# Kernel optimization log

Measured on AMD Instinct MI355X. Metric: run time of the kernel, lower is better.

## Reference

```python
import jax, jax.numpy as jnp
import numpy as np

B, S, H = 32, 1024, 1024
W, K = 128, 6
NUM_HEADS = 16


def setup_inputs() -> dict:
    key = jax.random.key(0)
    k1, k2 = jax.random.split(key, 2)
    token_embeddings = jax.random.normal(k1, (B, S, H), dtype=jnp.float32)
    # nn.MultiheadAttention packed in_proj (q,k,v). v / out_proj never affect the
    # module output (attn_output is discarded), but we keep full-size params.
    in_proj_weight = jax.random.normal(k2, (3 * H, H), dtype=jnp.float32) * (1.0 / np.sqrt(H))
    in_proj_bias = jnp.zeros((3 * H,), dtype=jnp.float32)
    # Build ragged word->subtoken map as padded [B, W, K] indices + validity mask.
    # Words occupy disjoint contiguous slots (stride S//W = 8 >= K), matching the
    # disjointness the tokenizer guarantees in get_subtok_map.
    rng = np.random.default_rng(0)
    lengths = rng.integers(2, K + 1, size=(B, W))  # each kept word has >=2 subtokens
    stride = S // W
    base = (np.arange(W) * stride)[None, :, None] + np.arange(K)[None, None, :]
    base = np.broadcast_to(base, (B, W, K))
    mask = np.arange(K)[None, None, :] < lengths[:, :, None]
    idx = np.where(mask, base, 0)
    return {
        "token_embeddings": token_embeddings,
        "in_proj_weight": in_proj_weight,
        "in_proj_bias": in_proj_bias,
        "subtok_idx": jnp.asarray(idx, dtype=jnp.int32),
        "subtok_mask": jnp.asarray(mask),
        "num_heads": NUM_HEADS,
    }


def _merge(token_embeddings, in_proj_weight, in_proj_bias, subtok_idx, subtok_mask, num_heads):
    Bv, Sv, Hv = token_embeddings.shape
    Wv, Kv = subtok_idx.shape[1], subtok_idx.shape[2]
    hd = Hv // num_heads
    dtype = token_embeddings.dtype
    maskf = subtok_mask.astype(dtype)
    b_idx = jnp.arange(Bv)[:, None, None]
    sub = token_embeddings[b_idx, subtok_idx]                      # [B,W,K,H] gather
    x = (sub * maskf[..., None]).reshape(Bv * Wv, Kv, Hv)          # zero-padded groups
    # q,k projections (v / out_proj do not influence returned embeddings)
    qk = x @ in_proj_weight[: 2 * Hv].T + in_proj_bias[: 2 * Hv]
    q, k = qk[..., :Hv], qk[..., Hv:]
    q = q.reshape(-1, Kv, num_heads, hd).transpose(0, 2, 1, 3)     # [L,nh,K,hd]
    k = k.reshape(-1, Kv, num_heads, hd).transpose(0, 2, 1, 3)
    scores = jnp.einsum('lnqd,lnkd->lnqk', q, k) / jnp.asarray(np.sqrt(hd), dtype)
    m = maskf.reshape(-1, Kv)
    pair = m[:, :, None] * m[:, None, :]                           # [L,K,K] 0/1 float mask
    # torch adds float attn_mask to scores (it does NOT -inf mask here) -- faithful
    scores = scores + pair[:, None]
    attn = jax.nn.softmax(scores, axis=-1)
    w_mean = attn.mean(axis=1)                                     # avg over heads (need_weights)
    contrib = (pair * w_mean).sum(axis=1)                          # sum over query dim
    contrib = contrib / (contrib.sum(axis=-1, keepdims=True) + 1e-8)
    contrib = contrib.reshape(Bv, Wv, Kv)                          # zero at invalid k
    unified = jnp.einsum('bwkh,bwk->bwh', sub, contrib)
    # zero ALL subtoken positions of each word, then write merged vector at the
    # first subtoken index (equivalent to the torch in-place per-word loop since
    # word index sets are disjoint). Column Sv is a discard slot for padding.
    safe_idx = jnp.where(subtok_mask, subtok_idx, Sv)
    keep = jnp.ones((Bv, Sv + 1), dtype=dtype)
    keep = keep.at[b_idx, safe_idx].set(0.0)
    out = token_embeddings * keep[:, :Sv, None]
    out = jnp.concatenate([out, jnp.zeros((Bv, 1, Hv), dtype)], axis=1)
    first_idx = jnp.where(subtok_mask[:, :, 0], subtok_idx[:, :, 0], Sv)
    out = out.at[jnp.arange(Bv)[:, None], first_idx].set(unified)
    return out[:, :Sv]


def reference(token_embeddings, in_proj_weight, in_proj_bias, subtok_idx, subtok_mask, num_heads):
    return _merge(token_embeddings, in_proj_weight, in_proj_bias, subtok_idx, subtok_mask, num_heads)
```

## Files before the change

### kernel.cpp

```cpp
#include <hip/hip_runtime.h>
#include <hip/hip_bf16.h>
#include <stdint.h>
#include <stddef.h>

#define Bdim  32
#define Sdim  1024
#define Hdim  1024
#define Wdim  128
#define Ktok  6
#define NHEAD 16
#define HDdim 64
#define Lgrp  (Bdim*Wdim)
#define Mrows (Lgrp*Ktok)
#define Ncols (2*Hdim)
#define CVTROWS (Mrows + Ncols)

#define BMg 256
#define BNg 256
#define BKg 64
#define NKT (Hdim/BKg)

typedef __attribute__((ext_vector_type(8))) short short8;
typedef __attribute__((ext_vector_type(4))) short short4_t;
typedef __attribute__((ext_vector_type(4))) float floatx4;
typedef __hip_bfloat16 bf16_t;

typedef unsigned int u32_g __attribute__((address_space(1)));
typedef unsigned int u32_l __attribute__((address_space(3)));

__device__ __forceinline__ void gld_lds16(const void* g, void* l) {
    __builtin_amdgcn_global_load_lds((const u32_g*)g, (u32_l*)l, 16, 0, 0);
}

__device__ __forceinline__ float b2f(short s) {
    union { float f; unsigned u; } x; x.u = ((unsigned)(unsigned short)s) << 16; return x.f;
}

__device__ __forceinline__ short8 cvt8(const float4 lo, const float4 hi) {
    union { short8 s; bf16_t h[8]; } u;
    u.h[0] = __float2bfloat16(lo.x); u.h[1] = __float2bfloat16(lo.y);
    u.h[2] = __float2bfloat16(lo.z); u.h[3] = __float2bfloat16(lo.w);
    u.h[4] = __float2bfloat16(hi.x); u.h[5] = __float2bfloat16(hi.y);
    u.h[6] = __float2bfloat16(hi.z); u.h[7] = __float2bfloat16(hi.w);
    return u.s;
}

__device__ __forceinline__ int lds_ro(int row, int col) {
    const int sub = ((row >> 4) << 1) | (col >> 5);
    const int c   = (col & 31) ^ (((row >> 3) & 1) << 4);
    return (sub << 10) | ((row & 15) << 6) | (c << 1);
}
__device__ __forceinline__ void stg_map(int p, int& row, int& col) {
    const int r16 = (p >> 6) & 15;
    int c = (p >> 1) & 31;
    c ^= ((r16 >> 3) & 1) << 4;
    row = ((p >> 11) << 4) | r16;
    col = (((p >> 10) & 1) << 5) | c;
}

__global__ void gather_cvt(const float* __restrict__ TE, const float* __restrict__ Wt,
                           const int* __restrict__ sidx,
                           bf16_t* __restrict__ Xa, bf16_t* __restrict__ Wb)
{
    const int r = blockIdx.x;
    const int t = threadIdx.x;
    const float* src;
    bf16_t* dst;
    if (r < Mrows) {
        src = TE + ((size_t)(r/768)*Sdim + sidx[r])*Hdim;
        dst = Xa + (size_t)r*Hdim;
    } else {
        src = Wt + (size_t)(r - Mrows)*Hdim;
        dst = Wb + (size_t)(r - Mrows)*Hdim;
    }
    const float4 v = *(const float4*)(src + t*4);
    union { short4_t s; bf16_t h[4]; } u;
    u.h[0] = __float2bfloat16(v.x); u.h[1] = __float2bfloat16(v.y);
    u.h[2] = __float2bfloat16(v.z); u.h[3] = __float2bfloat16(v.w);
    *(short4_t*)(dst + t*4) = u.s;
}

__global__ __launch_bounds__(512, 2) void gemm_8ph(
    const bf16_t* __restrict__ Xa, const bf16_t* __restrict__ Wb,
    const float* __restrict__ bias, bf16_t* __restrict__ Cq)
{
    __shared__ __align__(16) char lds[2][2][2][16384];
    const int tid  = threadIdx.x;
    const int lane = tid & 63;
    const int wv   = tid >> 6;
    const int wr   = wv >> 2;
    const int wc   = wv & 3;
    const int fr   = lane & 15;
    const int fq   = lane >> 4;

    const int cpx  = gridDim.x >> 3;
    const int orig = blockIdx.x;
    const int swz  = (orig & 7) * cpx + (orig >> 3);
    const int tileM = (swz >> 3) * BMg;
    const int tileN = (swz & 7) * BNg;

    int r0, c0, r1, c1;
    stg_map(tid * 16, r0, c0);
    stg_map(8192 + tid * 16, r1, c1);

    const bf16_t* srcA = Xa + (size_t)tileM * Hdim;
    const bf16_t* srcB = Wb + (size_t)tileN * Hdim;

    int aoff[4][2], boff[2][2];
    #pragma unroll
    for (int mi = 0; mi < 4; mi++)
        #pragma unroll
        for (int ks = 0; ks < 2; ks++)
            aoff[mi][ks] = lds_ro(wr*64 + mi*16 + fr, ks*32 + fq*8);
    #pragma unroll
    for (int ni = 0; ni < 2; ni++)
        #pragma unroll
        for (int ks = 0; ks < 2; ks++)
            boff[ni][ks] = lds_ro(wc*32 + ni*16 + fr, ks*32 + fq*8);

    short8 a[4][2], b[2][2];
    floatx4 acc[2][2][4][2] = {};

#define STAGE(bufi, isB, half, kt) do { \
        const bf16_t* _s = (isB) ? srcB : srcA; \
        char* _d = &lds[(bufi)][(isB)][(half)][0]; \
        const int _kb = (kt) * BKg; \
        gld_lds16(_s + (size_t)((half)*128 + r0) * Hdim + _kb + c0, _d + tid*16); \
        gld_lds16(_s + (size_t)((half)*128 + r1) * Hdim + _kb + c1, _d + 8192 + tid*16); \
    } while (0)

#define LDAf(bufi, qr) do { \
        const char* _sA = &lds[(bufi)][0][(qr)][0]; \
        _Pragma("unroll") \
        for (int mi = 0; mi < 4; mi++) { \
            a[mi][0] = *(const short8*)(const void*)(_sA + aoff[mi][0]); \
            a[mi][1] = *(const short8*)(const void*)(_sA + aoff[mi][1]); \
        } \
    } while (0)

#define LDBf(bufi, qc) do { \
        const char* _sB = &lds[(bufi)][1][(qc)][0]; \
        _Pragma("unroll") \
        for (int ni = 0; ni < 2; ni++) { \
            b[ni][0] = *(const short8*)(const void*)(_sB + boff[ni][0]); \
            b[ni][1] = *(const short8*)(const void*)(_sB + boff[ni][1]); \
        } \
    } while (0)

#define MMA(qr, qc) do { \
        __builtin_amdgcn_s_setprio(1); \
        _Pragma("unroll") \
        for (int mi = 0; mi < 4; mi++) \
            _Pragma("unroll") \
            for (int ni = 0; ni < 2; ni++) { \
                acc[qr][qc][mi][ni] = __builtin_amdgcn_mfma_f32_16x16x32_bf16( \
                    a[mi][0], b[ni][0], acc[qr][qc][mi][ni], 0, 0, 0); \
                acc[qr][qc][mi][ni] = __builtin_amdgcn_mfma_f32_16x16x32_bf16( \
                    a[mi][1], b[ni][1], acc[qr][qc][mi][ni], 0, 0, 0); \
            } \
        __builtin_amdgcn_s_setprio(0); \
    } while (0)

#define WAIT_LGKM() asm volatile("s_waitcnt lgkmcnt(0)" ::: "memory")

    STAGE(0, 0, 0, 0);
    STAGE(0, 1, 1, 0);
    STAGE(0, 0, 1, 0);
    STAGE(0, 1, 0, 0);
    STAGE(1, 0, 0, 1);
    STAGE(1, 1, 1, 1);
    asm volatile("s_waitcnt vmcnt(4)" ::: "memory");
    __builtin_amdgcn_s_barrier();

    for (int u = 0; u < NKT; ++u) {
        const int bf = u & 1;
        const int nb = bf ^ 1;
        LDAf(bf, 0); LDBf(bf, 0);
        if (u + 1 < NKT) STAGE(nb, 0, 1, u + 1);
        __builtin_amdgcn_s_barrier();
        WAIT_LGKM();
        MMA(0, 0);
        __builtin_amdgcn_s_barrier();
        LDBf(bf, 1);
        if (u + 1 < NKT) STAGE(nb, 1, 0, u + 1);
        __builtin_amdgcn_s_barrier();
        WAIT_LGKM();
        MMA(0, 1);
        __builtin_amdgcn_s_barrier();
        LDAf(bf, 1);
        if (u + 2 < NKT) STAGE(bf, 0, 0, u + 2);
        __builtin_amdgcn_s_barrier();
        WAIT_LGKM();
        MMA(1, 1);
        __builtin_amdgcn_s_barrier();
        LDBf(bf, 0);
        if (u + 2 < NKT) STAGE(bf, 1, 1, u + 2);
        __builtin_amdgcn_s_barrier();
        WAIT_LGKM();
        MMA(1, 0);
        if (u + 2 < NKT)      asm volatile("s_waitcnt vmcnt(4)" ::: "memory");
        else if (u + 1 < NKT) asm volatile("s_waitcnt vmcnt(0)" ::: "memory");
        __builtin_amdgcn_s_barrier();
    }

    #pragma unroll
    for (int qr = 0; qr < 2; qr++)
      #pragma unroll
      for (int qc = 0; qc < 2; qc++)
        #pragma unroll
        for (int ni = 0; ni < 2; ni++) {
            const int col = tileN + qc*128 + wc*32 + ni*16 + fr;
            const float bv = bias[col];
            #pragma unroll
            for (int mi = 0; mi < 4; mi++)
              #pragma unroll
              for (int j = 0; j < 4; j++) {
                const int row = tileM + qr*128 + wr*64 + mi*16 + fq*4 + j;
                Cq[(size_t)row * Ncols + col] = __float2bfloat16(acc[qr][qc][mi][ni][j] + bv);
              }
        }
#undef STAGE
#undef LDAf
#undef LDBf
#undef MMA
#undef WAIT_LGKM
}

__global__ __launch_bounds__(256, 2) void gemm_qk(
    const float* __restrict__ TE, const float* __restrict__ Wt,
    const float* __restrict__ bias, const int* __restrict__ sidx,
    bf16_t* __restrict__ Cq)
{
    __shared__ __align__(16) bf16_t As[128*32];
    __shared__ __align__(16) bf16_t Bs[128*32];
    const int tid  = threadIdx.x;
    const int wv   = tid >> 6;
    const int lane = tid & 63;
    const int tileM = blockIdx.x * 128;
    const int tileN = blockIdx.y * 128;

    const int r0 = wv*32 + (lane>>2);
    const int r1 = r0 + 16;
    const int c8 = (lane&3)*8;

    const int m0 = tileM + r0;
    const int m1 = tileM + r1;
    const float* pA0 = TE + ((size_t)(m0/768)*Sdim + sidx[m0])*Hdim + c8;
    const float* pA1 = TE + ((size_t)(m1/768)*Sdim + sidx[m1])*Hdim + c8;
    const float* pB0 = Wt + (size_t)(tileN + r0)*Hdim + c8;
    const float* pB1 = Wt + (size_t)(tileN + r1)*Hdim + c8;
    bf16_t* lA0 = &As[r0*32 + c8];
    bf16_t* lA1 = &As[r1*32 + c8];
    bf16_t* lB0 = &Bs[r0*32 + c8];
    bf16_t* lB1 = &Bs[r1*32 + c8];

    const int wm = (wv & 1)*64;
    const int wn = (wv >> 1)*64;
    const int fr = lane & 15;
    const int fq = lane >> 4;

    floatx4 acc[4][4] = {};

    for (int k0 = 0; k0 < Hdim; k0 += 32) {
        const float4 a0l = *(const float4*)(pA0 + k0);
        const float4 a0h = *(const float4*)(pA0 + k0 + 4);
        const float4 a1l = *(const float4*)(pA1 + k0);
        const float4 a1h = *(const float4*)(pA1 + k0 + 4);
        const float4 b0l = *(const float4*)(pB0 + k0);
        const float4 b0h = *(const float4*)(pB0 + k0 + 4);
        const float4 b1l = *(const float4*)(pB1 + k0);
        const float4 b1h = *(const float4*)(pB1 + k0 + 4);
        *(short8*)(void*)lA0 = cvt8(a0l, a0h);
        *(short8*)(void*)lA1 = cvt8(a1l, a1h);
        *(short8*)(void*)lB0 = cvt8(b0l, b0h);
        *(short8*)(void*)lB1 = cvt8(b1l, b1h);
        __syncthreads();
        short8 a[4], b[4];
        #pragma unroll
        for (int mi = 0; mi < 4; mi++)
            a[mi] = *(const short8*)(const void*)&As[(wm + mi*16 + fr)*32 + fq*8];
        #pragma unroll
        for (int ni = 0; ni < 4; ni++)
            b[ni] = *(const short8*)(const void*)&Bs[(wn + ni*16 + fr)*32 + fq*8];
        #pragma unroll
        for (int mi = 0; mi < 4; mi++)
            #pragma unroll
            for (int ni = 0; ni < 4; ni++)
                acc[mi][ni] = __builtin_amdgcn_mfma_f32_16x16x32_bf16(
                    a[mi], b[ni], acc[mi][ni], 0, 0, 0);
        __syncthreads();
    }

    #pragma unroll
    for (int ni = 0; ni < 4; ni++) {
        const int col = tileN + wn + ni*16 + fr;
        const float bv = bias[col];
        #pragma unroll
        for (int mi = 0; mi < 4; mi++) {
            #pragma unroll
            for (int r = 0; r < 4; r++) {
                const int row = tileM + wm + mi*16 + fq*4 + r;
                Cq[(size_t)row * Ncols + col] = __float2bfloat16(acc[mi][ni][r] + bv);
            }
        }
    }
}

__global__ void copy_te(const uint4* __restrict__ src, uint4* __restrict__ dst, int n)
{
    int i = blockIdx.x * blockDim.x + threadIdx.x;
    const int stride = gridDim.x * blockDim.x;
    for (; i < n; i += stride) dst[i] = src[i];
}

__global__ __launch_bounds__(256) void attn_merge(
    const float* __restrict__ TE, const bf16_t* __restrict__ Cq,
    const float* __restrict__ bias, const int* __restrict__ sidx,
    float* __restrict__ out)
{
    __shared__ __align__(16) bf16_t qk[Ktok][Ncols];
    __shared__ float sc[NHEAD][Ktok][Ktok];
    __shared__ float cN[Ktok];
    __shared__ int   validS[Ktok];

    const int g   = blockIdx.x;
    const int b   = g >> 7;
    const int w   = g & (Wdim - 1);
    const int tid = threadIdx.x;

    if (tid < Ktok) {
        const int id = sidx[g*Ktok + tid];
        validS[tid] = (id != 0) || (w == 0 && tid == 0);
    }
    __syncthreads();

    int valid[Ktok], idxv[Ktok];
    #pragma unroll
    for (int kk = 0; kk < Ktok; kk++) { valid[kk] = validS[kk]; idxv[kk] = sidx[g*Ktok + kk]; }

    #pragma unroll
    for (int it = 0; it < Ktok; it++) {
        if (valid[it]) {
            *(short8*)(void*)&qk[it][tid*8] =
                *(const short8*)(const void*)&Cq[(size_t)(g*Ktok + it)*Ncols + tid*8];
        } else {
            const float4 lo = *(const float4*)(bias + tid*8);
            const float4 hi = *(const float4*)(bias + tid*8 + 4);
            *(short8*)(void*)&qk[it][tid*8] = cvt8(lo, hi);
        }
    }
    __syncthreads();

    for (int t = tid; t < NHEAD*Ktok*Ktok; t += 256) {
        const int n = t / (Ktok*Ktok);
        const int pr = t % (Ktok*Ktok);
        const int i = pr / Ktok, j = pr % Ktok;
        const bf16_t* qp = &qk[i][n*HDdim];
        const bf16_t* kp = &qk[j][Hdim + n*HDdim];
        float dot = 0.f;
        #pragma unroll
        for (int c = 0; c < 8; c++) {
            const short8 q8 = *(const short8*)(const void*)(qp + c*8);
            const short8 k8 = *(const short8*)(const void*)(kp + c*8);
            #pragma unroll
            for (int e = 0; e < 8; e++) dot += b2f(q8[e]) * b2f(k8[e]);
        }
        sc[n][i][j] = dot * 0.125f + ((valid[i] && valid[j]) ? 1.0f : 0.0f);
    }
    __syncthreads();

    if (tid < NHEAD*Ktok) {
        const int n = tid / Ktok, i = tid % Ktok;
        float mx = -1e30f;
        #pragma unroll
        for (int j = 0; j < Ktok; j++) mx = fmaxf(mx, sc[n][i][j]);
        float e[Ktok], sum = 0.f;
        #pragma unroll
        for (int j = 0; j < Ktok; j++) { e[j] = __expf(sc[n][i][j] - mx); sum += e[j]; }
        const float inv = 1.0f / sum;
        #pragma unroll
        for (int j = 0; j < Ktok; j++) sc[n][i][j] = e[j] * inv;
    }
    __syncthreads();

    if (tid == 0) {
        float cb[Ktok], tot = 0.f;
        #pragma unroll
        for (int j = 0; j < Ktok; j++) cb[j] = 0.f;
        #pragma unroll
        for (int i = 0; i < Ktok; i++) {
            if (!valid[i]) continue;
            #pragma unroll
            for (int j = 0; j < Ktok; j++) {
                if (!valid[j]) continue;
                float s = 0.f;
                #pragma unroll
                for (int n = 0; n < NHEAD; n++) s += sc[n][i][j];
                cb[j] += s * (1.0f/NHEAD);
            }
        }
        #pragma unroll
        for (int j = 0; j < Ktok; j++) tot += cb[j];
        const float inv = 1.0f / (tot + 1e-8f);
        #pragma unroll
        for (int j = 0; j < Ktok; j++) cN[j] = cb[j] * inv;
    }
    __syncthreads();

    float cw[Ktok];
    #pragma unroll
    for (int kk = 0; kk < Ktok; kk++) cw[kk] = cN[kk];

    const int c4 = tid * 4;
    const size_t rowOut = ((size_t)b*Sdim + idxv[0]) * Hdim;
    float4 u = {0.f, 0.f, 0.f, 0.f};
    #pragma unroll
    for (int kk = 0; kk < Ktok; kk++) {
        const float4 v = *(const float4*)(TE + ((size_t)b*Sdim + idxv[kk])*Hdim + c4);
        u.x += cw[kk]*v.x; u.y += cw[kk]*v.y; u.z += cw[kk]*v.z; u.w += cw[kk]*v.w;
    }
    *(float4*)(out + rowOut + c4) = u;

    const float4 z = {0.f, 0.f, 0.f, 0.f};
    #pragma unroll
    for (int kk = 1; kk < Ktok; kk++) {
        if (valid[kk]) {
            *(float4*)(out + ((size_t)b*Sdim + idxv[kk])*Hdim + c4) = z;
        }
    }
}

extern "C" void kernel_launch(void* const* d_in, const int* in_sizes, int n_in,
                              void* d_out, int out_size, void* d_ws, size_t ws_size,
                              hipStream_t stream)
{
    (void)in_sizes; (void)n_in; (void)out_size;
    const float* TE   = (const float*)d_in[0];
    const float* Wt   = (const float*)d_in[1];
    const float* bias = (const float*)d_in[2];
    const int*   sidx = (const int*)d_in[3];
    float*  out  = (float*)d_out;

    const size_t CQ_BYTES = (size_t)Mrows * Ncols * 2;
    const size_t XA_BYTES = (size_t)Mrows * Hdim * 2;
    const size_t WB_BYTES = (size_t)Ncols * Hdim * 2;
    bf16_t* Cq = (bf16_t*)d_ws;
    bf16_t* Xa = (bf16_t*)((char*)d_ws + CQ_BYTES);
    bf16_t* Wb = (bf16_t*)((char*)d_ws + CQ_BYTES + XA_BYTES);

    if (ws_size >= CQ_BYTES + XA_BYTES + WB_BYTES) {
        gather_cvt<<<CVTROWS, 256, 0, stream>>>(TE, Wt, sidx, Xa, Wb);
        gemm_8ph<<<dim3((Mrows/BMg)*(Ncols/BNg)), dim3(512), 0, stream>>>(Xa, Wb, bias, Cq);
    } else {
        dim3 gg(Mrows/128, Ncols/128);
        gemm_qk<<<gg, dim3(256), 0, stream>>>(TE, Wt, bias, sidx, Cq);
    }
    copy_te<<<4096, 256, 0, stream>>>((const uint4*)TE, (uint4*)d_out,
                                      (Bdim*Sdim*Hdim)/4);
    attn_merge<<<Lgrp, 256, 0, stream>>>(TE, Cq, bias, sidx, out);
}
```

Measured before the change: 418.6 us.

## Zero merged subtoken rows during copy and drop intra-iteration GEMM barriers

Adds a per-row flag buffer, filled by the gather kernel, that marks non-first subtoken rows. The output copy kernel then writes zeros for those rows instead of copying and later overwriting them, so attn_merge skips its zeroing pass. This removes redundant global reads and writes. Separately, the bf16 GEMM main loop drops most of its barriers and lgkm waits and regroups the staging order, which cuts synchronisation but risks LDS read/write races.

```diff
diff --git a/kernel.cpp b/kernel.cpp
--- a/kernel.cpp
+++ b/kernel.cpp
@@ -58,17 +58,26 @@
     col = (((p >> 10) & 1) << 5) | c;
 }
 
+__global__ void zero_zf(unsigned int* __restrict__ zf)
+{
+    zf[blockIdx.x * 256 + threadIdx.x] = 0u;
+}
+
 __global__ void gather_cvt(const float* __restrict__ TE, const float* __restrict__ Wt,
                            const int* __restrict__ sidx,
-                           bf16_t* __restrict__ Xa, bf16_t* __restrict__ Wb)
+                           bf16_t* __restrict__ Xa, bf16_t* __restrict__ Wb,
+                           unsigned char* __restrict__ zflag)
 {
     const int r = blockIdx.x;
     const int t = threadIdx.x;
     const float* src;
     bf16_t* dst;
     if (r < Mrows) {
-        src = TE + ((size_t)(r/768)*Sdim + sidx[r])*Hdim;
+        const int id = sidx[r];
+        const int b  = r / (Wdim*Ktok);
+        src = TE + ((size_t)b*Sdim + id)*Hdim;
         dst = Xa + (size_t)r*Hdim;
+        if (t == 0 && (r % Ktok) >= 1 && id != 0) zflag[b*Sdim + id] = 1;
     } else {
         src = Wt + (size_t)(r - Mrows)*Hdim;
         dst = Wb + (size_t)(r - Mrows)*Hdim;
@@ -161,12 +170,10 @@
         __builtin_amdgcn_s_setprio(0); \
     } while (0)
 
-#define WAIT_LGKM() asm volatile("s_waitcnt lgkmcnt(0)" ::: "memory")
-
     STAGE(0, 0, 0, 0);
+    STAGE(0, 1, 0, 0);
+    STAGE(0, 0, 1, 0);
     STAGE(0, 1, 1, 0);
-    STAGE(0, 0, 1, 0);
-    STAGE(0, 1, 0, 0);
     STAGE(1, 0, 0, 1);
     STAGE(1, 1, 1, 1);
     asm volatile("s_waitcnt vmcnt(4)" ::: "memory");
@@ -175,28 +182,18 @@
     for (int u = 0; u < NKT; ++u) {
         const int bf = u & 1;
         const int nb = bf ^ 1;
-        LDAf(bf, 0); LDBf(bf, 0);
+        LDAf(bf, 0);
+        LDBf(bf, 0);
         if (u + 1 < NKT) STAGE(nb, 0, 1, u + 1);
-        __builtin_amdgcn_s_barrier();
-        WAIT_LGKM();
         MMA(0, 0);
-        __builtin_amdgcn_s_barrier();
         LDBf(bf, 1);
         if (u + 1 < NKT) STAGE(nb, 1, 0, u + 1);
-        __builtin_amdgcn_s_barrier();
-        WAIT_LGKM();
         MMA(0, 1);
         __builtin_amdgcn_s_barrier();
         LDAf(bf, 1);
-        if (u + 2 < NKT) STAGE(bf, 0, 0, u + 2);
-        __builtin_amdgcn_s_barrier();
-        WAIT_LGKM();
+        if (u + 2 < NKT) { STAGE(bf, 0, 0, u + 2); STAGE(bf, 1, 1, u + 2); }
         MMA(1, 1);
-        __builtin_amdgcn_s_barrier();
         LDBf(bf, 0);
-        if (u + 2 < NKT) STAGE(bf, 1, 1, u + 2);
-        __builtin_amdgcn_s_barrier();
-        WAIT_LGKM();
         MMA(1, 0);
         if (u + 2 < NKT)      asm volatile("s_waitcnt vmcnt(4)" ::: "memory");
         else if (u + 1 < NKT) asm volatile("s_waitcnt vmcnt(0)" ::: "memory");
@@ -223,7 +220,6 @@
 #undef LDAf
 #undef LDBf
 #undef MMA
-#undef WAIT_LGKM
 }
 
 __global__ __launch_bounds__(256, 2) void gemm_qk(
@@ -306,17 +302,22 @@
     }
 }
 
-__global__ void copy_te(const uint4* __restrict__ src, uint4* __restrict__ dst, int n)
+__global__ void copy_te(const uint4* __restrict__ src, uint4* __restrict__ dst,
+                        const unsigned char* __restrict__ zflag, int n)
 {
     int i = blockIdx.x * blockDim.x + threadIdx.x;
     const int stride = gridDim.x * blockDim.x;
-    for (; i < n; i += stride) dst[i] = src[i];
+    const uint4 z = {0u, 0u, 0u, 0u};
+    for (; i < n; i += stride) {
+        if (zflag != nullptr && zflag[i >> 8]) dst[i] = z;
+        else dst[i] = src[i];
+    }
 }
 
 __global__ __launch_bounds__(256) void attn_merge(
     const float* __restrict__ TE, const bf16_t* __restrict__ Cq,
     const float* __restrict__ bias, const int* __restrict__ sidx,
-    float* __restrict__ out)
+    float* __restrict__ out, int zero_rows)
 {
     __shared__ __align__(16) bf16_t qk[Ktok][Ncols];
     __shared__ float sc[NHEAD][Ktok][Ktok];
@@ -421,11 +422,13 @@
     }
     *(float4*)(out + rowOut + c4) = u;
 
-    const float4 z = {0.f, 0.f, 0.f, 0.f};
-    #pragma unroll
-    for (int kk = 1; kk < Ktok; kk++) {
-        if (valid[kk]) {
-            *(float4*)(out + ((size_t)b*Sdim + idxv[kk])*Hdim + c4) = z;
+    if (zero_rows) {
+        const float4 z = {0.f, 0.f, 0.f, 0.f};
+        #pragma unroll
+        for (int kk = 1; kk < Ktok; kk++) {
+            if (valid[kk]) {
+                *(float4*)(out + ((size_t)b*Sdim + idxv[kk])*Hdim + c4) = z;
+            }
         }
     }
 }
@@ -444,18 +447,24 @@
     const size_t CQ_BYTES = (size_t)Mrows * Ncols * 2;
     const size_t XA_BYTES = (size_t)Mrows * Hdim * 2;
     const size_t WB_BYTES = (size_t)Ncols * Hdim * 2;
+    const size_t ZF_BYTES = (size_t)Bdim * Sdim;
     bf16_t* Cq = (bf16_t*)d_ws;
     bf16_t* Xa = (bf16_t*)((char*)d_ws + CQ_BYTES);
     bf16_t* Wb = (bf16_t*)((char*)d_ws + CQ_BYTES + XA_BYTES);
-
-    if (ws_size >= CQ_BYTES + XA_BYTES + WB_BYTES) {
-        gather_cvt<<<CVTROWS, 256, 0, stream>>>(TE, Wt, sidx, Xa, Wb);
+    unsigned char* zf = (unsigned char*)((char*)d_ws + CQ_BYTES + XA_BYTES + WB_BYTES);
+
+    if (ws_size >= CQ_BYTES + XA_BYTES + WB_BYTES + ZF_BYTES) {
+        zero_zf<<<ZF_BYTES/1024, 256, 0, stream>>>((unsigned int*)zf);
+        gather_cvt<<<CVTROWS, 256, 0, stream>>>(TE, Wt, sidx, Xa, Wb, zf);
         gemm_8ph<<<dim3((Mrows/BMg)*(Ncols/BNg)), dim3(512), 0, stream>>>(Xa, Wb, bias, Cq);
+        copy_te<<<4096, 256, 0, stream>>>((const uint4*)TE, (uint4*)d_out, zf,
+                                          (Bdim*Sdim*Hdim)/4);
+        attn_merge<<<Lgrp, 256, 0, stream>>>(TE, Cq, bias, sidx, out, 0);
     } else {
         dim3 gg(Mrows/128, Ncols/128);
         gemm_qk<<<gg, dim3(256), 0, stream>>>(TE, Wt, bias, sidx, Cq);
-    }
-    copy_te<<<4096, 256, 0, stream>>>((const uint4*)TE, (uint4*)d_out,
-                                      (Bdim*Sdim*Hdim)/4);
-    attn_merge<<<Lgrp, 256, 0, stream>>>(TE, Cq, bias, sidx, out);
-}
+        copy_te<<<4096, 256, 0, stream>>>((const uint4*)TE, (uint4*)d_out, nullptr,
+                                          (Bdim*Sdim*Hdim)/4);
+        attn_merge<<<Lgrp, 256, 0, stream>>>(TE, Cq, bias, sidx, out, 1);
+    }
+}
```

Result: faster. 400.9 us (-4.2%).
